# Kernel tuning notes

Measured on AMD Instinct MI355X. Metric: run time of the kernel, lower is better.

## Reference

```python
import jax, jax.numpy as jnp
import numpy as np

# Level grid shapes: (T_i, H_i, W_i, C_i); K=(1,2,2) -> K_prod=4 folded into features
GRID_SIZES = [(120, 9, 16, 64), (60, 9, 16, 128), (30, 9, 16, 256)]
K_PROD = 4
C_OUT = 128
C_SUM = 64 + 128 + 256  # 448
INIT_SCALE = 0.001


def setup_inputs() -> dict:
    key = jax.random.key(0)
    ks = jax.random.split(key, 8)
    N, T, H, W = 2, 12, 36, 64
    inp = {
        'coor_t': jax.random.uniform(ks[0], (N, T), jnp.float32, -1.0, 1.0),
        'coor_h': jax.random.uniform(ks[1], (N, H), jnp.float32, -1.0, 1.0),
        'coor_w': jax.random.uniform(ks[2], (N, W), jnp.float32, -1.0, 1.0),
    }
    for i, (Tg, Hg, Wg, Cg) in enumerate(GRID_SIZES):
        inp[f'g{i}'] = jax.random.normal(ks[3 + i], (Tg * Hg * Wg, K_PROD * Cg), jnp.float32) * INIT_SCALE
    lim = 1.0 / np.sqrt(C_SUM)
    inp['lin_w'] = jax.random.uniform(ks[6], (C_OUT, C_SUM), jnp.float32, -lim, lim)
    inp['lin_b'] = jax.random.uniform(ks[7], (C_OUT,), jnp.float32, -lim, lim)
    return inp


def _prep_axis(c, S):
    # map [-1,1] -> [0, S-1] (align_corners=True), corner indices + frac weight
    x = (c + 1.0) * 0.5 * (S - 1)
    x0 = jnp.clip(jnp.floor(x), 0.0, S - 1)
    i0 = x0.astype(jnp.int32)
    i1 = jnp.clip(i0 + 1, 0, S - 1)
    return i0, i1, x - x0


def _interp3d(grid, coor_t, coor_h, coor_w):
    # grid: [Tg,Hg,Wg,Cf]; coords: [N,T],[N,H],[N,W] in [-1,1] -> [N,T,H,W,Cf]
    Tg, Hg, Wg, Cf = grid.shape
    t0, t1, ft = _prep_axis(coor_t, Tg)
    h0, h1, fh = _prep_axis(coor_h, Hg)
    w0, w1, fw = _prep_axis(coor_w, Wg)

    def g(ti, hi, wi):
        return grid[ti[:, :, None, None], hi[:, None, :, None], wi[:, None, None, :]]

    ft_ = ft[:, :, None, None, None]
    fh_ = fh[:, None, :, None, None]
    fw_ = fw[:, None, None, :, None]
    lo = ((g(t0, h0, w0) * (1 - fw_) + g(t0, h0, w1) * fw_) * (1 - fh_) +
          (g(t0, h1, w0) * (1 - fw_) + g(t0, h1, w1) * fw_) * fh_)
    hi = ((g(t1, h0, w0) * (1 - fw_) + g(t1, h0, w1) * fw_) * (1 - fh_) +
          (g(t1, h1, w0) * (1 - fw_) + g(t1, h1, w1) * fw_) * fh_)
    return lo * (1 - ft_) + hi * ft_


def reference(coor_t, coor_h, coor_w, g0, g1, g2, lin_w, lin_b):
    N, T = coor_t.shape
    H = coor_h.shape[1]
    W = coor_w.shape[1]
    grids = [g0, g1, g2]
    enc = []
    for i, (Tg, Hg, Wg, Cg) in enumerate(GRID_SIZES):
        weight = grids[i].reshape(Tg, Hg, Wg, K_PROD * Cg)
        e = _interp3d(weight, coor_t, coor_h, coor_w)  # [N,T,H,W,K*Cg]
        enc.append(e.reshape(N, T * H * W * K_PROD, Cg))
    feat = jnp.concatenate(enc, axis=-1)  # [N, T*H*W*K, 448]
    out = feat @ lin_w.T + lin_b          # [N, T*H*W*K, 128]
    return out.reshape(N, T, H, W, K_PROD * C_OUT)
```

## Files before the change

kernel.cpp:

```cpp
#include <hip/hip_runtime.h>

typedef __bf16 bf16x8 __attribute__((ext_vector_type(8)));
typedef __bf16 bf16x4 __attribute__((ext_vector_type(4)));
typedef float  f32x4  __attribute__((ext_vector_type(4)));

__device__ __forceinline__ bf16x8 pack8(float4 a, float4 b) {
    bf16x8 r;
    r[0] = (__bf16)a.x; r[1] = (__bf16)a.y; r[2] = (__bf16)a.z; r[3] = (__bf16)a.w;
    r[4] = (__bf16)b.x; r[5] = (__bf16)b.y; r[6] = (__bf16)b.z; r[7] = (__bf16)b.w;
    return r;
}

__global__ __launch_bounds__(256)
void proj_gemm_all(const float* __restrict__ g0, const float* __restrict__ g1,
                   const float* __restrict__ g2, const float* __restrict__ W,
                   const float* __restrict__ coor_t,
                   __bf16* __restrict__ P0, __bf16* __restrict__ P1,
                   __bf16* __restrict__ P2)
{
    __shared__ __bf16 As[128][40];
    __shared__ __bf16 Bs[128][40];

    const int b = blockIdx.x;
    const float* A; __bf16* P; int K, w_off, m0, Tg;
    if (b < 540)      { A = g0; P = P0; K = 64;  w_off = 0;   m0 = b * 128;         Tg = 120; }
    else if (b < 810) { A = g1; P = P1; K = 128; w_off = 64;  m0 = (b - 540) * 128; Tg = 60;  }
    else              { A = g2; P = P2; K = 256; w_off = 192; m0 = (b - 810) * 128; Tg = 30;  }

    {
        const int t_lo = m0 / 576;
        const int t_hi = (m0 + 127) / 576;
        bool need = false;
        for (int nt = 0; nt < 24; nt++) {
            float c  = coor_t[nt];
            float x0 = fminf(fmaxf(floorf((c + 1.0f) * 0.5f * (float)(Tg - 1)), 0.0f),
                             (float)(Tg - 1));
            int i0 = (int)x0;
            int i1 = (i0 + 1 < Tg - 1) ? (i0 + 1) : (Tg - 1);
            if (i0 == t_lo || i0 == t_hi || i1 == t_lo || i1 == t_hi) { need = true; break; }
        }
        if (!need) return;
    }

    const int tid  = threadIdx.x;
    const int wid  = tid >> 6;
    const int lane = tid & 63;
    const int lrow = lane & 15;
    const int lk   = (lane >> 4) * 8;

    f32x4 acc[2][8];
#pragma unroll
    for (int rt = 0; rt < 2; rt++)
#pragma unroll
        for (int ct = 0; ct < 8; ct++) acc[rt][ct] = f32x4{0.f, 0.f, 0.f, 0.f};

    const int srow = tid >> 1;
    const int half = tid & 1;

    for (int k0 = 0; k0 < K; k0 += 32) {
        {
            const float4* src = (const float4*)(A + (size_t)(m0 + srow) * K + k0 + half * 16);
            float4 f0 = src[0], f1 = src[1], f2 = src[2], f3 = src[3];
            *(bf16x8*)&As[srow][half * 16 + 0] = pack8(f0, f1);
            *(bf16x8*)&As[srow][half * 16 + 8] = pack8(f2, f3);
        }
        {
            const float4* src = (const float4*)(W + (size_t)srow * 448 + w_off + k0 + half * 16);
            float4 f0 = src[0], f1 = src[1], f2 = src[2], f3 = src[3];
            *(bf16x8*)&Bs[srow][half * 16 + 0] = pack8(f0, f1);
            *(bf16x8*)&Bs[srow][half * 16 + 8] = pack8(f2, f3);
        }
        __syncthreads();

        bf16x8 a[2], bfrag[8];
#pragma unroll
        for (int rt = 0; rt < 2; rt++)
            a[rt] = *(const bf16x8*)&As[wid * 32 + rt * 16 + lrow][lk];
#pragma unroll
        for (int ct = 0; ct < 8; ct++)
            bfrag[ct] = *(const bf16x8*)&Bs[ct * 16 + lrow][lk];
#pragma unroll
        for (int rt = 0; rt < 2; rt++)
#pragma unroll
            for (int ct = 0; ct < 8; ct++)
                acc[rt][ct] = __builtin_amdgcn_mfma_f32_16x16x32_bf16(a[rt], bfrag[ct], acc[rt][ct], 0, 0, 0);
        __syncthreads();
    }

#pragma unroll
    for (int rt = 0; rt < 2; rt++) {
        const int r0 = m0 + wid * 32 + rt * 16 + (lane >> 4) * 4;
#pragma unroll
        for (int ct = 0; ct < 8; ct++) {
            const int col = ct * 16 + lrow;
#pragma unroll
            for (int j = 0; j < 4; j++)
                P[(size_t)(r0 + j) * 128 + col] = (__bf16)acc[rt][ct][j];
        }
    }
}

__device__ __forceinline__ void addg(const bf16x4* __restrict__ P, int Tg, float c,
                                     int hw, int kc4, float* acc)
{
    float x  = (c + 1.0f) * 0.5f * (float)(Tg - 1);
    float x0 = fminf(fmaxf(floorf(x), 0.0f), (float)(Tg - 1));
    int   i0 = (int)x0;
    int   i1 = (i0 + 1 < Tg - 1) ? (i0 + 1) : (Tg - 1);
    float f  = x - x0;
    bf16x4 lo = P[(i0 * 144 + hw) * 128 + kc4];
    bf16x4 hi = P[(i1 * 144 + hw) * 128 + kc4];
    float omf = 1.0f - f;
#pragma unroll
    for (int j = 0; j < 4; j++)
        acc[j] += (float)lo[j] * omf + (float)hi[j] * f;
}

__global__ __launch_bounds__(256)
void tmix(const bf16x4* __restrict__ P0, const bf16x4* __restrict__ P1,
          const bf16x4* __restrict__ P2, const float* __restrict__ coor_t,
          bf16x4* __restrict__ G)
{
    int v   = blockIdx.x * 256 + threadIdx.x;
    int kc4 = v & 127;
    int w   = (v >> 7) & 15;
    int r   = v >> 11;
    int h   = r % 9;
    int nt  = r / 9;
    float c = coor_t[nt];
    int  hw = h * 16 + w;

    float acc[4] = {0.f, 0.f, 0.f, 0.f};
    addg(P0, 120, c, hw, kc4, acc);
    addg(P1,  60, c, hw, kc4, acc);
    addg(P2,  30, c, hw, kc4, acc);

    bf16x4 o;
#pragma unroll
    for (int j = 0; j < 4; j++) o[j] = (__bf16)acc[j];
    G[v] = o;
}

__global__ __launch_bounds__(256)
void finalk(const bf16x4* __restrict__ G, const float* __restrict__ coor_h,
            const float* __restrict__ coor_w, const float* __restrict__ lin_b,
            float4* __restrict__ out)
{
    int v   = blockIdx.x * 256 + threadIdx.x;
    int kc4 = v & 127;
    int w   = (v >> 7) & 63;
    int r   = v >> 13;
    int h   = r % 36;
    int nt  = r / 36;
    int n   = nt / 12;

    float ch = coor_h[n * 36 + h];
    float cw = coor_w[n * 64 + w];

    float xh  = (ch + 1.0f) * 0.5f * 8.0f;
    float xh0 = fminf(fmaxf(floorf(xh), 0.0f), 8.0f);
    int   h0  = (int)xh0;
    int   h1  = (h0 + 1 < 8) ? (h0 + 1) : 8;
    float fh  = xh - xh0;
    float xw  = (cw + 1.0f) * 0.5f * 15.0f;
    float xw0 = fminf(fmaxf(floorf(xw), 0.0f), 15.0f);
    int   w0  = (int)xw0;
    int   w1  = (w0 + 1 < 15) ? (w0 + 1) : 15;
    float fw  = xw - xw0;

    int base = nt * 18432 + kc4;
    bf16x4 g00 = G[base + (h0 * 16 + w0) * 128];
    bf16x4 g01 = G[base + (h0 * 16 + w1) * 128];
    bf16x4 g10 = G[base + (h1 * 16 + w0) * 128];
    bf16x4 g11 = G[base + (h1 * 16 + w1) * 128];

    float4 b = ((const float4*)lin_b)[kc4 & 31];
    float ofw = 1.0f - fw, ofh = 1.0f - fh;

    float4 o;
    o.x = ((float)g00[0] * ofw + (float)g01[0] * fw) * ofh + ((float)g10[0] * ofw + (float)g11[0] * fw) * fh + b.x;
    o.y = ((float)g00[1] * ofw + (float)g01[1] * fw) * ofh + ((float)g10[1] * ofw + (float)g11[1] * fw) * fh + b.y;
    o.z = ((float)g00[2] * ofw + (float)g01[2] * fw) * ofh + ((float)g10[2] * ofw + (float)g11[2] * fw) * fh + b.z;
    o.w = ((float)g00[3] * ofw + (float)g01[3] * fw) * ofh + ((float)g10[3] * ofw + (float)g11[3] * fw) * fh + b.w;
    out[v] = o;
}

extern "C" void kernel_launch(void* const* d_in, const int* in_sizes, int n_in,
                              void* d_out, int out_size, void* d_ws, size_t ws_size,
                              hipStream_t stream)
{
    const float* coor_t = (const float*)d_in[0];
    const float* coor_h = (const float*)d_in[1];
    const float* coor_w = (const float*)d_in[2];
    const float* g0     = (const float*)d_in[3];
    const float* g1     = (const float*)d_in[4];
    const float* g2     = (const float*)d_in[5];
    const float* lin_w  = (const float*)d_in[6];
    const float* lin_b  = (const float*)d_in[7];
    float* out = (float*)d_out;

    char* ws = (char*)d_ws;
    __bf16* P0 = (__bf16*)(ws + 0);
    __bf16* P1 = (__bf16*)(ws + 17694720);
    __bf16* P2 = (__bf16*)(ws + 26542080);
    __bf16* G  = (__bf16*)(ws + 30965760);

    proj_gemm_all<<<945, 256, 0, stream>>>(g0, g1, g2, lin_w, coor_t, P0, P1, P2);

    tmix<<<1728, 256, 0, stream>>>((const bf16x4*)P0, (const bf16x4*)P1,
                                   (const bf16x4*)P2, coor_t, (bf16x4*)G);

    finalk<<<27648, 256, 0, stream>>>((const bf16x4*)G, coor_h, coor_w, lin_b,
                                      (float4*)out);
}
```

Measured before the change: 192.9 us.

## Interpolate grids along time before GEMM and fuse temporal mix into projection

Temporal interpolation now happens first: each GEMM block gathers the two time slices for its nt, blends them in fp32, and runs one K=448 GEMM producing G directly. This replaces the projection of every needed grid row at all three levels plus a separate tmix pass, removing the P0/P1/P2 intermediates and one launch. In exchange the GEMM uses only 216 blocks with 64-row tiles, which may underfill the device. The final kernel also switches to nontemporal stores for the output.

After: 186.0 us. 1.04x faster.

```diff
diff --git a/kernel.cpp b/kernel.cpp
--- a/kernel.cpp
+++ b/kernel.cpp
@@ -12,35 +12,16 @@
 }
 
 __global__ __launch_bounds__(256)
-void proj_gemm_all(const float* __restrict__ g0, const float* __restrict__ g1,
-                   const float* __restrict__ g2, const float* __restrict__ W,
-                   const float* __restrict__ coor_t,
-                   __bf16* __restrict__ P0, __bf16* __restrict__ P1,
-                   __bf16* __restrict__ P2)
+void gemmG(const float* __restrict__ g0, const float* __restrict__ g1,
+           const float* __restrict__ g2, const float* __restrict__ W,
+           const float* __restrict__ coor_t, __bf16* __restrict__ G)
 {
-    __shared__ __bf16 As[128][40];
+    __shared__ __bf16 As[64][40];
     __shared__ __bf16 Bs[128][40];
 
-    const int b = blockIdx.x;
-    const float* A; __bf16* P; int K, w_off, m0, Tg;
-    if (b < 540)      { A = g0; P = P0; K = 64;  w_off = 0;   m0 = b * 128;         Tg = 120; }
-    else if (b < 810) { A = g1; P = P1; K = 128; w_off = 64;  m0 = (b - 540) * 128; Tg = 60;  }
-    else              { A = g2; P = P2; K = 256; w_off = 192; m0 = (b - 810) * 128; Tg = 30;  }
-
-    {
-        const int t_lo = m0 / 576;
-        const int t_hi = (m0 + 127) / 576;
-        bool need = false;
-        for (int nt = 0; nt < 24; nt++) {
-            float c  = coor_t[nt];
-            float x0 = fminf(fmaxf(floorf((c + 1.0f) * 0.5f * (float)(Tg - 1)), 0.0f),
-                             (float)(Tg - 1));
-            int i0 = (int)x0;
-            int i1 = (i0 + 1 < Tg - 1) ? (i0 + 1) : (Tg - 1);
-            if (i0 == t_lo || i0 == t_hi || i1 == t_lo || i1 == t_hi) { need = true; break; }
-        }
-        if (!need) return;
-    }
+    const int m0 = blockIdx.x * 64;
+    const int nt = m0 / 576;
+    const float c = coor_t[nt];
 
     const int tid  = threadIdx.x;
     const int wid  = tid >> 6;
@@ -48,103 +29,78 @@
     const int lrow = lane & 15;
     const int lk   = (lane >> 4) * 8;
 
-    f32x4 acc[2][8];
-#pragma unroll
-    for (int rt = 0; rt < 2; rt++)
-#pragma unroll
-        for (int ct = 0; ct < 8; ct++) acc[rt][ct] = f32x4{0.f, 0.f, 0.f, 0.f};
+    const int srow = tid >> 2;
+    const int q    = tid & 3;
+    const int rem  = (m0 % 576) + srow;
+    const int hw   = rem >> 2;
+    const int kp   = rem & 3;
 
-    const int srow = tid >> 1;
+    const int bcol = tid >> 1;
     const int half = tid & 1;
 
-    for (int k0 = 0; k0 < K; k0 += 32) {
+    f32x4 acc[8];
+#pragma unroll
+    for (int ct = 0; ct < 8; ct++) acc[ct] = f32x4{0.f, 0.f, 0.f, 0.f};
+
+    for (int k0 = 0; k0 < 448; k0 += 32) {
+        const float* gp; int off, Cg, Tg;
+        if (k0 < 64)       { gp = g0; off = 0;   Cg = 64;  Tg = 120; }
+        else if (k0 < 192) { gp = g1; off = 64;  Cg = 128; Tg = 60;  }
+        else               { gp = g2; off = 192; Cg = 256; Tg = 30;  }
+
+        float x  = (c + 1.0f) * 0.5f * (float)(Tg - 1);
+        float x0 = fminf(fmaxf(floorf(x), 0.0f), (float)(Tg - 1));
+        int   i0 = (int)x0;
+        int   i1 = (i0 + 1 < Tg - 1) ? (i0 + 1) : (Tg - 1);
+        float ft = x - x0;
+        float omf = 1.0f - ft;
+
         {
-            const float4* src = (const float4*)(A + (size_t)(m0 + srow) * K + k0 + half * 16);
-            float4 f0 = src[0], f1 = src[1], f2 = src[2], f3 = src[3];
-            *(bf16x8*)&As[srow][half * 16 + 0] = pack8(f0, f1);
-            *(bf16x8*)&As[srow][half * 16 + 8] = pack8(f2, f3);
+            const size_t ch = (size_t)(k0 - off) + q * 8;
+            const float4* s0 = (const float4*)(gp + ((size_t)(i0 * 144 + hw) * 4 + kp) * Cg + ch);
+            const float4* s1 = (const float4*)(gp + ((size_t)(i1 * 144 + hw) * 4 + kp) * Cg + ch);
+            float4 a0 = s0[0], a1 = s0[1];
+            float4 b0 = s1[0], b1 = s1[1];
+            float4 v0, v1;
+            v0.x = a0.x * omf + b0.x * ft; v0.y = a0.y * omf + b0.y * ft;
+            v0.z = a0.z * omf + b0.z * ft; v0.w = a0.w * omf + b0.w * ft;
+            v1.x = a1.x * omf + b1.x * ft; v1.y = a1.y * omf + b1.y * ft;
+            v1.z = a1.z * omf + b1.z * ft; v1.w = a1.w * omf + b1.w * ft;
+            *(bf16x8*)&As[srow][q * 8] = pack8(v0, v1);
         }
         {
-            const float4* src = (const float4*)(W + (size_t)srow * 448 + w_off + k0 + half * 16);
+            const float4* src = (const float4*)(W + (size_t)bcol * 448 + k0 + half * 16);
             float4 f0 = src[0], f1 = src[1], f2 = src[2], f3 = src[3];
-            *(bf16x8*)&Bs[srow][half * 16 + 0] = pack8(f0, f1);
-            *(bf16x8*)&Bs[srow][half * 16 + 8] = pack8(f2, f3);
+            *(bf16x8*)&Bs[bcol][half * 16 + 0] = pack8(f0, f1);
+            *(bf16x8*)&Bs[bcol][half * 16 + 8] = pack8(f2, f3);
         }
         __syncthreads();
 
-        bf16x8 a[2], bfrag[8];
-#pragma unroll
-        for (int rt = 0; rt < 2; rt++)
-            a[rt] = *(const bf16x8*)&As[wid * 32 + rt * 16 + lrow][lk];
+        bf16x8 a = *(const bf16x8*)&As[wid * 16 + lrow][lk];
+        bf16x8 bfrag[8];
 #pragma unroll
         for (int ct = 0; ct < 8; ct++)
             bfrag[ct] = *(const bf16x8*)&Bs[ct * 16 + lrow][lk];
 #pragma unroll
-        for (int rt = 0; rt < 2; rt++)
-#pragma unroll
-            for (int ct = 0; ct < 8; ct++)
-                acc[rt][ct] = __builtin_amdgcn_mfma_f32_16x16x32_bf16(a[rt], bfrag[ct], acc[rt][ct], 0, 0, 0);
+        for (int ct = 0; ct < 8; ct++)
+            acc[ct] = __builtin_amdgcn_mfma_f32_16x16x32_bf16(a, bfrag[ct], acc[ct], 0, 0, 0);
         __syncthreads();
     }
 
+    const int r0 = m0 + wid * 16 + (lane >> 4) * 4;
 #pragma unroll
-    for (int rt = 0; rt < 2; rt++) {
-        const int r0 = m0 + wid * 32 + rt * 16 + (lane >> 4) * 4;
+    for (int ct = 0; ct < 8; ct++) {
+        const int col = ct * 16 + lrow;
 #pragma unroll
-        for (int ct = 0; ct < 8; ct++) {
-            const int col = ct * 16 + lrow;
-#pragma unroll
-            for (int j = 0; j < 4; j++)
-                P[(size_t)(r0 + j) * 128 + col] = (__bf16)acc[rt][ct][j];
-        }
+        for (int j = 0; j < 4; j++)
+            G[(size_t)(r0 + j) * 128 + col] = (__bf16)acc[ct][j];
     }
-}
-
-__device__ __forceinline__ void addg(const bf16x4* __restrict__ P, int Tg, float c,
-                                     int hw, int kc4, float* acc)
-{
-    float x  = (c + 1.0f) * 0.5f * (float)(Tg - 1);
-    float x0 = fminf(fmaxf(floorf(x), 0.0f), (float)(Tg - 1));
-    int   i0 = (int)x0;
-    int   i1 = (i0 + 1 < Tg - 1) ? (i0 + 1) : (Tg - 1);
-    float f  = x - x0;
-    bf16x4 lo = P[(i0 * 144 + hw) * 128 + kc4];
-    bf16x4 hi = P[(i1 * 144 + hw) * 128 + kc4];
-    float omf = 1.0f - f;
-#pragma unroll
-    for (int j = 0; j < 4; j++)
-        acc[j] += (float)lo[j] * omf + (float)hi[j] * f;
-}
-
-__global__ __launch_bounds__(256)
-void tmix(const bf16x4* __restrict__ P0, const bf16x4* __restrict__ P1,
-          const bf16x4* __restrict__ P2, const float* __restrict__ coor_t,
-          bf16x4* __restrict__ G)
-{
-    int v   = blockIdx.x * 256 + threadIdx.x;
-    int kc4 = v & 127;
-    int w   = (v >> 7) & 15;
-    int r   = v >> 11;
-    int h   = r % 9;
-    int nt  = r / 9;
-    float c = coor_t[nt];
-    int  hw = h * 16 + w;
-
-    float acc[4] = {0.f, 0.f, 0.f, 0.f};
-    addg(P0, 120, c, hw, kc4, acc);
-    addg(P1,  60, c, hw, kc4, acc);
-    addg(P2,  30, c, hw, kc4, acc);
-
-    bf16x4 o;
-#pragma unroll
-    for (int j = 0; j < 4; j++) o[j] = (__bf16)acc[j];
-    G[v] = o;
 }
 
 __global__ __launch_bounds__(256)
 void finalk(const bf16x4* __restrict__ G, const float* __restrict__ coor_h,
             const float* __restrict__ coor_w, const float* __restrict__ lin_b,
-            float4* __restrict__ out)
+            f32x4* __restrict__ out)
 {
     int v   = blockIdx.x * 256 + threadIdx.x;
     int kc4 = v & 127;
@@ -177,12 +133,12 @@
     float4 b = ((const float4*)lin_b)[kc4 & 31];
     float ofw = 1.0f - fw, ofh = 1.0f - fh;
 
-    float4 o;
-    o.x = ((float)g00[0] * ofw + (float)g01[0] * fw) * ofh + ((float)g10[0] * ofw + (float)g11[0] * fw) * fh + b.x;
-    o.y = ((float)g00[1] * ofw + (float)g01[1] * fw) * ofh + ((float)g10[1] * ofw + (float)g11[1] * fw) * fh + b.y;
-    o.z = ((float)g00[2] * ofw + (float)g01[2] * fw) * ofh + ((float)g10[2] * ofw + (float)g11[2] * fw) * fh + b.z;
-    o.w = ((float)g00[3] * ofw + (float)g01[3] * fw) * ofh + ((float)g10[3] * ofw + (float)g11[3] * fw) * fh + b.w;
-    out[v] = o;
+    f32x4 o;
+    o[0] = ((float)g00[0] * ofw + (float)g01[0] * fw) * ofh + ((float)g10[0] * ofw + (float)g11[0] * fw) * fh + b.x;
+    o[1] = ((float)g00[1] * ofw + (float)g01[1] * fw) * ofh + ((float)g10[1] * ofw + (float)g11[1] * fw) * fh + b.y;
+    o[2] = ((float)g00[2] * ofw + (float)g01[2] * fw) * ofh + ((float)g10[2] * ofw + (float)g11[2] * fw) * fh + b.z;
+    o[3] = ((float)g00[3] * ofw + (float)g01[3] * fw) * ofh + ((float)g10[3] * ofw + (float)g11[3] * fw) * fh + b.w;
+    __builtin_nontemporal_store(o, &out[v]);
 }
 
 extern "C" void kernel_launch(void* const* d_in, const int* in_sizes, int n_in,
@@ -197,19 +153,11 @@
     const float* g2     = (const float*)d_in[5];
     const float* lin_w  = (const float*)d_in[6];
     const float* lin_b  = (const float*)d_in[7];
-    float* out = (float*)d_out;
 
-    char* ws = (char*)d_ws;
-    __bf16* P0 = (__bf16*)(ws + 0);
-    __bf16* P1 = (__bf16*)(ws + 17694720);
-    __bf16* P2 = (__bf16*)(ws + 26542080);
-    __bf16* G  = (__bf16*)(ws + 30965760);
+    __bf16* G = (__bf16*)d_ws;
 
-    proj_gemm_all<<<945, 256, 0, stream>>>(g0, g1, g2, lin_w, coor_t, P0, P1, P2);
-
-    tmix<<<1728, 256, 0, stream>>>((const bf16x4*)P0, (const bf16x4*)P1,
-                                   (const bf16x4*)P2, coor_t, (bf16x4*)G);
+    gemmG<<<216, 256, 0, stream>>>(g0, g1, g2, lin_w, coor_t, G);
 
     finalk<<<27648, 256, 0, stream>>>((const bf16x4*)G, coor_h, coor_w, lin_b,
-                                      (float4*)out);
+                                      (f32x4*)d_out);
 }
```
